# Optimization experiments

Hardware: AMD Instinct MI355X
Metric: run time of the kernel (lower is better)

Reference implementation:

```python
import jax, jax.numpy as jnp
import numpy as np

H = 128      # hidden_units
L = 200      # maxlen
B = 2048     # batch of sequences
E = 8        # num_experts
SW = 64      # switch hidden dim


def setup_inputs() -> dict:
    key = jax.random.key(0)
    ks = jax.random.split(key, 16)
    s = 0.05
    inp = {
        "x": jax.random.normal(ks[0], (B, L, H), jnp.float32),
        "x_real": jax.random.normal(ks[1], (1, L, H), jnp.float32),
        "user_embedding": jax.random.normal(ks[2], (1, H), jnp.float32),
        # uexpert: conv1d(H,H,1) -> relu -> conv1d(H,H,1); weights [out,in]
        "uW1": jax.random.normal(ks[3], (H, H), jnp.float32) * s,
        "ub1": jax.random.normal(ks[4], (H,), jnp.float32) * s,
        "uW2": jax.random.normal(ks[5], (H, H), jnp.float32) * s,
        "ub2": jax.random.normal(ks[6], (H,), jnp.float32) * s,
        # stacked expert weights [E, out, in]
        "eW1": jax.random.normal(ks[7], (E, H, H), jnp.float32) * s,
        "eb1": jax.random.normal(ks[8], (E, H), jnp.float32) * s,
        "eW2": jax.random.normal(ks[9], (E, H, H), jnp.float32) * s,
        "eb2": jax.random.normal(ks[10], (E, H), jnp.float32) * s,
        # switch MLP: H -> SW -> E
        "sW1": jax.random.normal(ks[11], (SW, H), jnp.float32) * s,
        "sb1": jax.random.normal(ks[12], (SW,), jnp.float32) * s,
        "sW2": jax.random.normal(ks[13], (E, SW), jnp.float32) * s,
        "sb2": jax.random.normal(ks[14], (E,), jnp.float32) * s,
    }
    return inp


def _ffn(x, W1, b1, W2, b2):
    # conv1d(k=1) -> (dropout: identity at eval) -> relu -> conv1d(k=1) -> dropout
    h = jax.nn.relu(jnp.einsum("blh,oh->blo", x, W1) + b1)
    return jnp.einsum("blh,oh->blo", h, W2) + b2


def reference(x, x_real, user_embedding, uW1, ub1, uW2, ub2,
              eW1, eb1, eW2, eb2, sW1, sb1, sW2, sb2):
    # client_rep == 'avg': mean over the sequence of x_real -> [H]
    x_input = jnp.mean(x_real[0], axis=0)
    # switch MLP with ReLU on all but last layer
    h = jax.nn.relu(x_input @ sW1.T + sb1)
    logits = h @ sW2.T + sb2                      # [E]
    route_prob = jax.nn.softmax(logits, axis=-1)
    route = jnp.argmax(route_prob, axis=-1)       # scalar expert index
    out_prob_max = route_prob[route]
    # selected expert branch
    expert_out = _ffn(x, eW1[route], eb1[route], eW2[route], eb2[route])
    # always-on uexpert branch
    uexpert_out = _ffn(x, uW1, ub1, uW2, ub2)
    final_output = expert_out + uexpert_out       # [B, L, H]
    return (final_output, route, out_prob_max)
```

## Files before the change

### kernel.cpp

```cpp
#include <hip/hip_runtime.h>

#define HD 128
#define LSEQ 200
#define BATCH 2048
#define NE 8
#define SWH 64

#define BM 32
#define LDX 136
#define LDH 264
#define NTILES ((BATCH * LSEQ) / BM)
#define GRID 512

typedef float f32x4 __attribute__((ext_vector_type(4)));
typedef __bf16 bf16x4 __attribute__((ext_vector_type(4)));
typedef __bf16 bf16x8 __attribute__((ext_vector_type(8)));

#define BAR() do {                                          \
    asm volatile("s_waitcnt lgkmcnt(0)" ::: "memory");      \
    __builtin_amdgcn_sched_barrier(0);                      \
    __builtin_amdgcn_s_barrier();                           \
    __builtin_amdgcn_sched_barrier(0);                      \
} while (0)

static __device__ __forceinline__ unsigned short f2bf(float f) {
    union { float f; unsigned u; } v; v.f = f;
    unsigned u = v.u;
    u += 0x7fffu + ((u >> 16) & 1u);
    return (unsigned short)(u >> 16);
}

__global__ void prep_route(const float* __restrict__ x_real,
                           const float* __restrict__ sW1, const float* __restrict__ sb1,
                           const float* __restrict__ sW2, const float* __restrict__ sb2,
                           const float* __restrict__ uW1, const float* __restrict__ ub1,
                           const float* __restrict__ uW2, const float* __restrict__ ub2,
                           const float* __restrict__ eW1, const float* __restrict__ eb1,
                           const float* __restrict__ eW2, const float* __restrict__ eb2,
                           float* __restrict__ out_tail,
                           unsigned short* __restrict__ W1c, unsigned short* __restrict__ W2c,
                           float* __restrict__ b1c, float* __restrict__ b2s) {
    __shared__ float part[256];
    __shared__ float xm[HD];
    __shared__ float hsw[SWH];
    __shared__ float logits[NE];
    __shared__ int route_s;
    const int t = threadIdx.x;

    {
        int col = t & 127, half = t >> 7;
        float s = 0.f;
        for (int l = half * 100; l < half * 100 + 100; ++l) s += x_real[l * HD + col];
        part[t] = s;
    }
    __syncthreads();
    if (t < HD) xm[t] = (part[t] + part[t + 128]) * (1.0f / LSEQ);
    __syncthreads();
    if (t < SWH) {
        float s = sb1[t];
        for (int k = 0; k < HD; ++k) s += xm[k] * sW1[t * HD + k];
        hsw[t] = s > 0.f ? s : 0.f;
    }
    __syncthreads();
    if (t < NE) {
        float s = sb2[t];
        for (int k = 0; k < SWH; ++k) s += hsw[k] * sW2[t * SWH + k];
        logits[t] = s;
    }
    __syncthreads();
    if (t == 0) {
        float mx = logits[0]; int am = 0;
        for (int e = 1; e < NE; ++e) if (logits[e] > mx) { mx = logits[e]; am = e; }
        float den = 0.f;
        for (int e = 0; e < NE; ++e) den += __expf(logits[e] - mx);
        route_s = am;
        if (blockIdx.x == 0) {
            out_tail[0] = (float)am;
            out_tail[1] = 1.0f / den;
        }
    }
    __syncthreads();
    const int r = route_s;

    const int i = blockIdx.x * 256 + t;
    if (i < 2 * HD * HD) {
        int o = i >> 7, k = i & 127;
        float v1 = (o < HD) ? uW1[o * HD + k] : eW1[r * HD * HD + (o - HD) * HD + k];
        W1c[i] = f2bf(v1);
        int o2 = i >> 8, j = i & 255;
        float v2 = (j < HD) ? uW2[o2 * HD + j] : eW2[r * HD * HD + o2 * HD + (j - HD)];
        W2c[i] = f2bf(v2);
    }
    if (i < 2 * HD) b1c[i] = (i < HD) ? ub1[i] : eb1[r * HD + (i - HD)];
    if (i < HD)     b2s[i] = ub2[i] + eb2[r * HD + i];
}

__global__ __launch_bounds__(256, 2)
void moe_main(const float* __restrict__ x,
              const unsigned short* __restrict__ W1c, const unsigned short* __restrict__ W2c,
              const float* __restrict__ b1c, const float* __restrict__ b2s,
              float* __restrict__ out) {
    __shared__ __align__(16) unsigned short xs[2][BM * LDX];
    __shared__ __align__(16) unsigned short hs[2][BM * LDH];

    const int t = threadIdx.x;
    const int lane = t & 63;
    const int w = t >> 6;
    const int l16 = lane & 15;
    const int lq = lane >> 4;
    const int ncb = w * 64;
    const int ncb2 = w * 32;

    bf16x8 w1[4][4];
    bf16x8 w2[8][2];
#pragma unroll
    for (int ks = 0; ks < 4; ++ks)
#pragma unroll
        for (int ht = 0; ht < 4; ++ht)
            w1[ks][ht] = *(const bf16x8*)&W1c[(ncb + ht * 16 + l16) * HD + ks * 32 + lq * 8];
#pragma unroll
    for (int ks = 0; ks < 8; ++ks)
#pragma unroll
        for (int ct = 0; ct < 2; ++ct)
            w2[ks][ct] = *(const bf16x8*)&W2c[(ncb2 + ct * 16 + l16) * 256 + ks * 32 + lq * 8];

    f32x4 bias1v[4], bias2v[2];
#pragma unroll
    for (int ht = 0; ht < 4; ++ht) bias1v[ht] = *(const f32x4*)&b1c[ncb + ht * 16 + lq * 4];
#pragma unroll
    for (int ct = 0; ct < 2; ++ct) bias2v[ct] = *(const f32x4*)&b2s[ncb2 + ct * 16 + lq * 4];

    const int srow0 = t >> 5;
    const int sc4 = (t & 31) * 4;

    const int t0 = blockIdx.x;
    float4 pv[4];
    {
        const float4* x4 = (const float4*)(x + (size_t)t0 * (BM * HD));
#pragma unroll
        for (int i = 0; i < 4; ++i) pv[i] = x4[t + i * 256];
    }
#pragma unroll
    for (int i = 0; i < 4; ++i) {
        bf16x4 b;
        b[0] = (__bf16)pv[i].x; b[1] = (__bf16)pv[i].y;
        b[2] = (__bf16)pv[i].z; b[3] = (__bf16)pv[i].w;
        *(bf16x4*)&xs[0][(srow0 + i * 8) * LDX + sc4] = b;
    }
    if (t0 + GRID < NTILES) {
        const float4* x4 = (const float4*)(x + (size_t)(t0 + GRID) * (BM * HD));
#pragma unroll
        for (int i = 0; i < 4; ++i) pv[i] = x4[t + i * 256];
    }
    BAR();

    int b = 1, q = 0;
    for (int tile = t0; tile < NTILES + GRID; tile += GRID) {
        if (tile < NTILES) {
            const unsigned short* xsr = xs[b ^ 1];
            unsigned short* hsw_ = hs[q];
            f32x4 acc1[4][2] = {};
#pragma unroll
            for (int ks = 0; ks < 4; ++ks) {
                const int kofs = ks * 32 + lq * 8;
                bf16x8 xf[2];
#pragma unroll
                for (int tt = 0; tt < 2; ++tt)
                    xf[tt] = *(const bf16x8*)&xsr[(tt * 16 + l16) * LDX + kofs];
#pragma unroll
                for (int ht = 0; ht < 4; ++ht)
#pragma unroll
                    for (int tt = 0; tt < 2; ++tt)
                        acc1[ht][tt] = __builtin_amdgcn_mfma_f32_16x16x32_bf16(
                            w1[ks][ht], xf[tt], acc1[ht][tt], 0, 0, 0);
            }
#pragma unroll
            for (int ht = 0; ht < 4; ++ht)
#pragma unroll
                for (int tt = 0; tt < 2; ++tt) {
                    bf16x4 hv;
#pragma unroll
                    for (int r = 0; r < 4; ++r) {
                        float v = acc1[ht][tt][r] + bias1v[ht][r];
                        hv[r] = (__bf16)(v > 0.f ? v : 0.f);
                    }
                    *(bf16x4*)&hsw_[(tt * 16 + l16) * LDH + ncb + ht * 16 + lq * 4] = hv;
                }
        }

        if (tile > t0) {
            const unsigned short* hsr = hs[q ^ 1];
            f32x4 acc2[2][2] = {};
#pragma unroll
            for (int ks = 0; ks < 8; ++ks) {
                const int kofs = ks * 32 + lq * 8;
                bf16x8 hf[2];
#pragma unroll
                for (int tt = 0; tt < 2; ++tt)
                    hf[tt] = *(const bf16x8*)&hsr[(tt * 16 + l16) * LDH + kofs];
#pragma unroll
                for (int ct = 0; ct < 2; ++ct)
#pragma unroll
                    for (int tt = 0; tt < 2; ++tt)
                        acc2[ct][tt] = __builtin_amdgcn_mfma_f32_16x16x32_bf16(
                            w2[ks][ct], hf[tt], acc2[ct][tt], 0, 0, 0);
            }
            float* outp = out + (size_t)(tile - GRID) * (BM * HD);
#pragma unroll
            for (int ct = 0; ct < 2; ++ct)
#pragma unroll
                for (int tt = 0; tt < 2; ++tt) {
                    f32x4 o;
#pragma unroll
                    for (int r = 0; r < 4; ++r) o[r] = acc2[ct][tt][r] + bias2v[ct][r];
                    *(f32x4*)&outp[(size_t)(tt * 16 + l16) * HD + ncb2 + ct * 16 + lq * 4] = o;
                }
        }

        if (tile + GRID < NTILES) {
            unsigned short* xsw = xs[b];
#pragma unroll
            for (int i = 0; i < 4; ++i) {
                bf16x4 bb;
                bb[0] = (__bf16)pv[i].x; bb[1] = (__bf16)pv[i].y;
                bb[2] = (__bf16)pv[i].z; bb[3] = (__bf16)pv[i].w;
                *(bf16x4*)&xsw[(srow0 + i * 8) * LDX + sc4] = bb;
            }
            if (tile + 2 * GRID < NTILES) {
                const float4* x4 = (const float4*)(x + (size_t)(tile + 2 * GRID) * (BM * HD));
#pragma unroll
                for (int i = 0; i < 4; ++i) pv[i] = x4[t + i * 256];
            }
        }

        BAR();
        b ^= 1; q ^= 1;
    }
}

extern "C" void kernel_launch(void* const* d_in, const int* in_sizes, int n_in,
                              void* d_out, int out_size, void* d_ws, size_t ws_size,
                              hipStream_t stream) {
    const float* x      = (const float*)d_in[0];
    const float* x_real = (const float*)d_in[1];
    const float* uW1 = (const float*)d_in[3];
    const float* ub1 = (const float*)d_in[4];
    const float* uW2 = (const float*)d_in[5];
    const float* ub2 = (const float*)d_in[6];
    const float* eW1 = (const float*)d_in[7];
    const float* eb1 = (const float*)d_in[8];
    const float* eW2 = (const float*)d_in[9];
    const float* eb2 = (const float*)d_in[10];
    const float* sW1 = (const float*)d_in[11];
    const float* sb1 = (const float*)d_in[12];
    const float* sW2 = (const float*)d_in[13];
    const float* sb2 = (const float*)d_in[14];
    float* out = (float*)d_out;

    char* ws = (char*)d_ws;
    unsigned short* W1c = (unsigned short*)(ws + 64);
    unsigned short* W2c = (unsigned short*)(ws + 64 + 65536);
    float* b1c = (float*)(ws + 64 + 131072);
    float* b2s = (float*)(ws + 64 + 131072 + 1024);

    prep_route<<<128, 256, 0, stream>>>(x_real, sW1, sb1, sW2, sb2,
                                        uW1, ub1, uW2, ub2, eW1, eb1, eW2, eb2,
                                        out + (size_t)BATCH * LSEQ * HD,
                                        W1c, W2c, b1c, b2s);
    moe_main<<<GRID, 256, 0, stream>>>(x, W1c, W2c, b1c, b2s, out);
}
```

Before: 99.89 us.

## Warp-specialize blocks into GEMM1 and GEMM2 wave groups with 512 threads

Doubles block size to 512 threads and splits waves into two roles: four waves compute the first FFN layer into shared memory while the other four load and convert x tiles and compute the second layer plus output stores. Each wave now holds only one weight set in registers, which lowers register pressure. Bias loads move from registers to per-iteration global reads. The intent is to overlap the two GEMM stages across wave groups, at the cost of possible load imbalance between the groups. Launch bounds of (512,4) may force register spills.

```diff
diff --git a/kernel.cpp b/kernel.cpp
--- a/kernel.cpp
+++ b/kernel.cpp
@@ -11,6 +11,7 @@
 #define LDH 264
 #define NTILES ((BATCH * LSEQ) / BM)
 #define GRID 512
+#define KITER 25
 
 typedef float f32x4 __attribute__((ext_vector_type(4)));
 typedef __bf16 bf16x4 __attribute__((ext_vector_type(4)));
@@ -95,7 +96,7 @@
     if (i < HD)     b2s[i] = ub2[i] + eb2[r * HD + i];
 }
 
-__global__ __launch_bounds__(256, 2)
+__global__ __launch_bounds__(512, 4)
 void moe_main(const float* __restrict__ x,
               const unsigned short* __restrict__ W1c, const unsigned short* __restrict__ W2c,
               const float* __restrict__ b1c, const float* __restrict__ b2s,
@@ -108,131 +109,132 @@
     const int w = t >> 6;
     const int l16 = lane & 15;
     const int lq = lane >> 4;
-    const int ncb = w * 64;
-    const int ncb2 = w * 32;
-
-    bf16x8 w1[4][4];
-    bf16x8 w2[8][2];
-#pragma unroll
-    for (int ks = 0; ks < 4; ++ks)
-#pragma unroll
-        for (int ht = 0; ht < 4; ++ht)
-            w1[ks][ht] = *(const bf16x8*)&W1c[(ncb + ht * 16 + l16) * HD + ks * 32 + lq * 8];
-#pragma unroll
-    for (int ks = 0; ks < 8; ++ks)
-#pragma unroll
-        for (int ct = 0; ct < 2; ++ct)
-            w2[ks][ct] = *(const bf16x8*)&W2c[(ncb2 + ct * 16 + l16) * 256 + ks * 32 + lq * 8];
-
-    f32x4 bias1v[4], bias2v[2];
-#pragma unroll
-    for (int ht = 0; ht < 4; ++ht) bias1v[ht] = *(const f32x4*)&b1c[ncb + ht * 16 + lq * 4];
-#pragma unroll
-    for (int ct = 0; ct < 2; ++ct) bias2v[ct] = *(const f32x4*)&b2s[ncb2 + ct * 16 + lq * 4];
-
-    const int srow0 = t >> 5;
-    const int sc4 = (t & 31) * 4;
+    const bool isG1 = (w >= 4);
+
+    bf16x8 wt[16];
+    if (isG1) {
+        const int ncb = (w - 4) * 64;
+#pragma unroll
+        for (int ks = 0; ks < 4; ++ks)
+#pragma unroll
+            for (int ht = 0; ht < 4; ++ht)
+                wt[ks * 4 + ht] = *(const bf16x8*)&W1c[(ncb + ht * 16 + l16) * HD + ks * 32 + lq * 8];
+    } else {
+        const int ncb2 = w * 32;
+#pragma unroll
+        for (int ks = 0; ks < 8; ++ks)
+#pragma unroll
+            for (int ct = 0; ct < 2; ++ct)
+                wt[ks * 2 + ct] = *(const bf16x8*)&W2c[(ncb2 + ct * 16 + l16) * 256 + ks * 32 + lq * 8];
+    }
 
     const int t0 = blockIdx.x;
-    float4 pv[4];
-    {
+
+    float4 lv[4];
+    if (!isG1) {
         const float4* x4 = (const float4*)(x + (size_t)t0 * (BM * HD));
 #pragma unroll
-        for (int i = 0; i < 4; ++i) pv[i] = x4[t + i * 256];
-    }
-#pragma unroll
-    for (int i = 0; i < 4; ++i) {
-        bf16x4 b;
-        b[0] = (__bf16)pv[i].x; b[1] = (__bf16)pv[i].y;
-        b[2] = (__bf16)pv[i].z; b[3] = (__bf16)pv[i].w;
-        *(bf16x4*)&xs[0][(srow0 + i * 8) * LDX + sc4] = b;
-    }
-    if (t0 + GRID < NTILES) {
-        const float4* x4 = (const float4*)(x + (size_t)(t0 + GRID) * (BM * HD));
-#pragma unroll
-        for (int i = 0; i < 4; ++i) pv[i] = x4[t + i * 256];
+        for (int i = 0; i < 4; ++i) lv[i] = x4[t + i * 256];
+#pragma unroll
+        for (int i = 0; i < 4; ++i) {
+            int idx = t + i * 256;
+            bf16x4 b;
+            b[0] = (__bf16)lv[i].x; b[1] = (__bf16)lv[i].y;
+            b[2] = (__bf16)lv[i].z; b[3] = (__bf16)lv[i].w;
+            *(bf16x4*)&xs[0][(idx >> 5) * LDX + (idx & 31) * 4] = b;
+        }
+        const float4* x4b = (const float4*)(x + (size_t)(t0 + GRID) * (BM * HD));
+#pragma unroll
+        for (int i = 0; i < 4; ++i) lv[i] = x4b[t + i * 256];
     }
     BAR();
 
     int b = 1, q = 0;
-    for (int tile = t0; tile < NTILES + GRID; tile += GRID) {
-        if (tile < NTILES) {
-            const unsigned short* xsr = xs[b ^ 1];
-            unsigned short* hsw_ = hs[q];
-            f32x4 acc1[4][2] = {};
-#pragma unroll
-            for (int ks = 0; ks < 4; ++ks) {
-                const int kofs = ks * 32 + lq * 8;
-                bf16x8 xf[2];
-#pragma unroll
-                for (int tt = 0; tt < 2; ++tt)
-                    xf[tt] = *(const bf16x8*)&xsr[(tt * 16 + l16) * LDX + kofs];
-#pragma unroll
-                for (int ht = 0; ht < 4; ++ht)
+    for (int it = 0; it <= KITER; ++it) {
+        if (isG1) {
+            if (it <= KITER - 1) {
+                const int ncb = (w - 4) * 64;
+                const unsigned short* xsr = xs[b ^ 1];
+                unsigned short* hsw_ = hs[q];
+                f32x4 acc[4][2] = {};
+#pragma unroll
+                for (int ks = 0; ks < 4; ++ks) {
+                    const int kofs = ks * 32 + lq * 8;
+                    bf16x8 xf[2];
 #pragma unroll
                     for (int tt = 0; tt < 2; ++tt)
-                        acc1[ht][tt] = __builtin_amdgcn_mfma_f32_16x16x32_bf16(
-                            w1[ks][ht], xf[tt], acc1[ht][tt], 0, 0, 0);
-            }
-#pragma unroll
-            for (int ht = 0; ht < 4; ++ht)
-#pragma unroll
-                for (int tt = 0; tt < 2; ++tt) {
-                    bf16x4 hv;
-#pragma unroll
-                    for (int r = 0; r < 4; ++r) {
-                        float v = acc1[ht][tt][r] + bias1v[ht][r];
-                        hv[r] = (__bf16)(v > 0.f ? v : 0.f);
+                        xf[tt] = *(const bf16x8*)&xsr[(tt * 16 + l16) * LDX + kofs];
+#pragma unroll
+                    for (int ht = 0; ht < 4; ++ht)
+#pragma unroll
+                        for (int tt = 0; tt < 2; ++tt)
+                            acc[ht][tt] = __builtin_amdgcn_mfma_f32_16x16x32_bf16(
+                                wt[ks * 4 + ht], xf[tt], acc[ht][tt], 0, 0, 0);
+                }
+#pragma unroll
+                for (int ht = 0; ht < 4; ++ht) {
+                    f32x4 b1v = *(const f32x4*)&b1c[ncb + ht * 16 + lq * 4];
+#pragma unroll
+                    for (int tt = 0; tt < 2; ++tt) {
+                        bf16x4 hv;
+#pragma unroll
+                        for (int rr = 0; rr < 4; ++rr) {
+                            float v = acc[ht][tt][rr] + b1v[rr];
+                            hv[rr] = (__bf16)(v > 0.f ? v : 0.f);
+                        }
+                        *(bf16x4*)&hsw_[(tt * 16 + l16) * LDH + ncb + ht * 16 + lq * 4] = hv;
                     }
-                    *(bf16x4*)&hsw_[(tt * 16 + l16) * LDH + ncb + ht * 16 + lq * 4] = hv;
-                }
+                }
+            }
+        } else {
+            if (it <= KITER - 2) {
+                unsigned short* xsw = xs[b];
+#pragma unroll
+                for (int i = 0; i < 4; ++i) {
+                    int idx = t + i * 256;
+                    bf16x4 bb;
+                    bb[0] = (__bf16)lv[i].x; bb[1] = (__bf16)lv[i].y;
+                    bb[2] = (__bf16)lv[i].z; bb[3] = (__bf16)lv[i].w;
+                    *(bf16x4*)&xsw[(idx >> 5) * LDX + (idx & 31) * 4] = bb;
+                }
+            }
+            if (it <= KITER - 3) {
+                const float4* x4n = (const float4*)(x + (size_t)(t0 + (it + 2) * GRID) * (BM * HD));
+#pragma unroll
+                for (int i = 0; i < 4; ++i) lv[i] = x4n[t + i * 256];
+            }
+            if (it >= 1) {
+                const int ncb2 = w * 32;
+                const unsigned short* hsr = hs[q ^ 1];
+                f32x4 acc[2][2] = {};
+#pragma unroll
+                for (int ks = 0; ks < 8; ++ks) {
+                    const int kofs = ks * 32 + lq * 8;
+                    bf16x8 hf[2];
+#pragma unroll
+                    for (int tt = 0; tt < 2; ++tt)
+                        hf[tt] = *(const bf16x8*)&hsr[(tt * 16 + l16) * LDH + kofs];
+#pragma unroll
+                    for (int ct = 0; ct < 2; ++ct)
+#pragma unroll
+                        for (int tt = 0; tt < 2; ++tt)
+                            acc[ct][tt] = __builtin_amdgcn_mfma_f32_16x16x32_bf16(
+                                wt[ks * 2 + ct], hf[tt], acc[ct][tt], 0, 0, 0);
+                }
+                float* outp = out + (size_t)(t0 + (it - 1) * GRID) * (BM * HD);
+#pragma unroll
+                for (int ct = 0; ct < 2; ++ct) {
+                    f32x4 b2v = *(const f32x4*)&b2s[ncb2 + ct * 16 + lq * 4];
+#pragma unroll
+                    for (int tt = 0; tt < 2; ++tt) {
+                        f32x4 o;
+#pragma unroll
+                        for (int rr = 0; rr < 4; ++rr) o[rr] = acc[ct][tt][rr] + b2v[rr];
+                        *(f32x4*)&outp[(size_t)(tt * 16 + l16) * HD + ncb2 + ct * 16 + lq * 4] = o;
+                    }
+                }
+            }
         }
-
-        if (tile > t0) {
-            const unsigned short* hsr = hs[q ^ 1];
-            f32x4 acc2[2][2] = {};
-#pragma unroll
-            for (int ks = 0; ks < 8; ++ks) {
-                const int kofs = ks * 32 + lq * 8;
-                bf16x8 hf[2];
-#pragma unroll
-                for (int tt = 0; tt < 2; ++tt)
-                    hf[tt] = *(const bf16x8*)&hsr[(tt * 16 + l16) * LDH + kofs];
-#pragma unroll
-                for (int ct = 0; ct < 2; ++ct)
-#pragma unroll
-                    for (int tt = 0; tt < 2; ++tt)
-                        acc2[ct][tt] = __builtin_amdgcn_mfma_f32_16x16x32_bf16(
-                            w2[ks][ct], hf[tt], acc2[ct][tt], 0, 0, 0);
-            }
-            float* outp = out + (size_t)(tile - GRID) * (BM * HD);
-#pragma unroll
-            for (int ct = 0; ct < 2; ++ct)
-#pragma unroll
-                for (int tt = 0; tt < 2; ++tt) {
-                    f32x4 o;
-#pragma unroll
-                    for (int r = 0; r < 4; ++r) o[r] = acc2[ct][tt][r] + bias2v[ct][r];
-                    *(f32x4*)&outp[(size_t)(tt * 16 + l16) * HD + ncb2 + ct * 16 + lq * 4] = o;
-                }
-        }
-
-        if (tile + GRID < NTILES) {
-            unsigned short* xsw = xs[b];
-#pragma unroll
-            for (int i = 0; i < 4; ++i) {
-                bf16x4 bb;
-                bb[0] = (__bf16)pv[i].x; bb[1] = (__bf16)pv[i].y;
-                bb[2] = (__bf16)pv[i].z; bb[3] = (__bf16)pv[i].w;
-                *(bf16x4*)&xsw[(srow0 + i * 8) * LDX + sc4] = bb;
-            }
-            if (tile + 2 * GRID < NTILES) {
-                const float4* x4 = (const float4*)(x + (size_t)(tile + 2 * GRID) * (BM * HD));
-#pragma unroll
-                for (int i = 0; i < 4; ++i) pv[i] = x4[t + i * 256];
-            }
-        }
-
         BAR();
         b ^= 1; q ^= 1;
     }
@@ -267,5 +269,5 @@
                                         uW1, ub1, uW2, ub2, eW1, eb1, eW2, eb2,
                                         out + (size_t)BATCH * LSEQ * HD,
                                         W1c, W2c, b1c, b2s);
-    moe_main<<<GRID, 256, 0, stream>>>(x, W1c, W2c, b1c, b2s, out);
-}
+    moe_main<<<GRID, 512, 0, stream>>>(x, W1c, W2c, b1c, b2s, out);
+}
```

After: 228.1 us. +128.3%, slower.
